# Optimization experiments

Measured on AMD Instinct MI355X. Metric: run time of the kernel, lower is better.

The kernel has to match this reference:

```python
import jax, jax.numpy as jnp
import numpy as np

N_NODES = 100000
N_EDGES = 3200000
N_FEAT = 128
EMBED = 20
N_CLASSES = 10
N_GRAPHS = 64


def setup_inputs() -> dict:
    key = jax.random.key(0)
    ks = jax.random.split(key, 8)
    x = jax.random.normal(ks[0], (N_NODES, N_FEAT), dtype=jnp.float32)
    edge_index = jax.random.randint(ks[1], (2, N_EDGES), 0, N_NODES, dtype=jnp.int64)
    edge_weights = jax.random.uniform(ks[2], (N_EDGES,), dtype=jnp.float32)
    batch = jnp.sort(jax.random.randint(ks[3], (N_NODES,), 0, N_GRAPHS, dtype=jnp.int64))
    # GCNConv parameters (glorot-ish scale) and final linear layer
    W = jax.random.normal(ks[4], (N_FEAT, EMBED), dtype=jnp.float32) * (1.0 / np.sqrt(N_FEAT))
    b = jnp.zeros((EMBED,), dtype=jnp.float32)
    lin_W = jax.random.normal(ks[5], (2 * EMBED, N_CLASSES), dtype=jnp.float32) * (1.0 / np.sqrt(2 * EMBED))
    lin_b = jnp.zeros((N_CLASSES,), dtype=jnp.float32)
    return {"x": x, "edge_index": edge_index, "edge_weights": edge_weights,
            "batch": batch, "W": W, "b": b, "lin_W": lin_W, "lin_b": lin_b}


def reference(x, edge_index, edge_weights, batch, W, b, lin_W, lin_b):
    N = x.shape[0]
    # --- GCNConv with self-loops and symmetric normalization (PyG semantics) ---
    loops = jnp.arange(N, dtype=edge_index.dtype)
    src = jnp.concatenate([edge_index[0], loops])
    dst = jnp.concatenate([edge_index[1], loops])
    w = jnp.concatenate([edge_weights, jnp.ones((N,), dtype=edge_weights.dtype)])
    deg = jax.ops.segment_sum(w, dst, num_segments=N)  # degree at targets
    dinv = jnp.where(deg > 0, jax.lax.rsqrt(deg), 0.0)
    norm = dinv[src] * w * dinv[dst]  # [E+N]
    xw = x @ W  # [N, EMBED]
    msg = xw[src] * norm[:, None]  # gather + scale
    out1 = jax.ops.segment_sum(msg, dst, num_segments=N) + b  # scatter-add
    # --- L2 normalize per node (F.normalize p=2 dim=1, eps=1e-12), then ReLU ---
    nrm = jnp.sqrt(jnp.sum(out1 * out1, axis=1, keepdims=True))
    embed = jax.nn.relu(out1 / jnp.maximum(nrm, 1e-12))
    # --- global max / mean pool per graph ---
    mx = jax.ops.segment_max(embed, batch, num_segments=N_GRAPHS)
    mx = jnp.where(jnp.isfinite(mx), mx, 0.0)  # empty graphs -> 0
    cnt = jax.ops.segment_sum(jnp.ones((N,), dtype=embed.dtype), batch, num_segments=N_GRAPHS)
    mean = jax.ops.segment_sum(embed, batch, num_segments=N_GRAPHS) / jnp.maximum(cnt, 1.0)[:, None]
    pooled = jnp.concatenate([mx, mean], axis=-1)  # [G, 2*EMBED]
    return pooled @ lin_W + lin_b
```

## Files before the change

### kernel.cpp

```cpp
#include <hip/hip_runtime.h>
#include <hip/hip_fp16.h>

#define NN 100000
#define NE 3200000
#define NF 128
#define EM 20
#define NC 10
#define NG 64

#define NB 782
#define CAPB 4608
#define T 4096
#define SBLK 1024

__global__ __launch_bounds__(SBLK) void k_scatter(
        const int* __restrict__ src, const int* __restrict__ dst,
        const float* __restrict__ w, int* __restrict__ gcursor,
        uint2* __restrict__ barr) {
    __shared__ unsigned int cnt[1024];
    __shared__ unsigned int off[1024];
    __shared__ unsigned int gbase[NB];
    __shared__ unsigned int wsum[16];
    __shared__ uint2 staged[T];
    __shared__ unsigned short bkt[T];
    int tid = threadIdx.x;
    long E0 = (long)blockIdx.x * T;
    int tot = (int)min((long)T, (long)NE - E0);
    cnt[tid] = 0;
    __syncthreads();
    unsigned int dreg[T / SBLK];
#pragma unroll
    for (int k = 0; k < T / SBLK; ++k) {
        int e = k * SBLK + tid;
        dreg[k] = 0;
        if (e < tot) {
            dreg[k] = (unsigned)dst[E0 + e];
            atomicAdd(&cnt[dreg[k] >> 7], 1u);
        }
    }
    __syncthreads();
    {
        int lane = tid & 63, wv = tid >> 6;
        unsigned int v = cnt[tid];
        unsigned int s = v;
#pragma unroll
        for (int o = 1; o < 64; o <<= 1) {
            unsigned int t = __shfl_up(s, o);
            if (lane >= o) s += t;
        }
        if (lane == 63) wsum[wv] = s;
        __syncthreads();
        if (tid == 0) {
            unsigned int a = 0;
#pragma unroll
            for (int i = 0; i < 16; ++i) { unsigned int t = wsum[i]; wsum[i] = a; a += t; }
        }
        __syncthreads();
        off[tid] = wsum[wv] + s - v;
    }
    __syncthreads();
    if (tid < NB) {
        unsigned int c = cnt[tid];
        gbase[tid] = c ? (unsigned int)atomicAdd(&gcursor[tid], (int)c) : 0u;
        cnt[tid] = 0;
    }
    __syncthreads();
#pragma unroll
    for (int k = 0; k < T / SBLK; ++k) {
        int e = k * SBLK + tid;
        if (e < tot) {
            long ge = E0 + e;
            unsigned int d = dreg[k];
            unsigned int b = d >> 7;
            unsigned int slot = atomicAdd(&cnt[b], 1u);
            unsigned int pos = off[b] + slot;
            staged[pos] = make_uint2((((unsigned)src[ge]) << 7) | (d & 127u),
                                     __float_as_uint(w[ge]));
            bkt[pos] = (unsigned short)b;
        }
    }
    __syncthreads();
    for (int i = tid; i < tot; i += SBLK) {
        unsigned int b = bkt[i];
        unsigned int gpos = gbase[b] + ((unsigned)i - off[b]);
        if (gpos < CAPB) barr[(size_t)b * CAPB + gpos] = staged[i];
    }
}

__global__ void k_degb(const int* __restrict__ gcursor, const uint2* __restrict__ barr,
                       float* __restrict__ dinv) {
    __shared__ float dacc[128];
    int bk = blockIdx.x, tid = threadIdx.x;
    if (tid < 128) dacc[tid] = 0.f;
    __syncthreads();
    int cntb = min(gcursor[bk], CAPB);
    const uint2* row = barr + (size_t)bk * CAPB;
    for (int i = tid; i < cntb; i += 1024) {
        uint2 r = row[i];
        atomicAdd(&dacc[r.x & 127u], __uint_as_float(r.y));
    }
    __syncthreads();
    if (tid < 128) {
        int gd = bk * 128 + tid;
        if (gd < NN) dinv[gd] = rsqrtf(1.0f + dacc[tid]);
    }
}

__global__ void k_xw(const float* __restrict__ x, const float* __restrict__ W,
                     const float* __restrict__ dinv,
                     __half* __restrict__ xwhA, __half* __restrict__ xwhB) {
    __shared__ float xs[64 * 129];
    __shared__ float Ws[NF * EM];
    int base = blockIdx.x * 64;
    for (int i = threadIdx.x; i < NF * EM; i += 256) Ws[i] = W[i];
    const float4* xg = (const float4*)(x + (size_t)base * NF);
    for (int v = threadIdx.x; v < 64 * NF / 4; v += 256) {
        int fidx = v * 4;
        size_t gidx = (size_t)base * NF + fidx;
        float4 val = (gidx + 3 < (size_t)NN * NF) ? xg[v] : make_float4(0.f, 0.f, 0.f, 0.f);
        int r = fidx / NF, c = fidx % NF;
        float* p = xs + r * 129 + c;
        p[0] = val.x; p[1] = val.y; p[2] = val.z; p[3] = val.w;
    }
    __syncthreads();
    int n = threadIdx.x & 63;
    int jg = threadIdx.x >> 6;
    int j0 = jg * 5;
    if (base + n >= NN) return;
    float acc[5] = {0.f, 0.f, 0.f, 0.f, 0.f};
    const float* xr = xs + n * 129;
#pragma unroll 4
    for (int k = 0; k < NF; ++k) {
        float xv = xr[k];
        const float* wr = Ws + k * EM + j0;
#pragma unroll
        for (int jj = 0; jj < 5; ++jj) acc[jj] = fmaf(xv, wr[jj], acc[jj]);
    }
    float dv = dinv[base + n];
#pragma unroll
    for (int jj = 0; jj < 5; ++jj) {
        int j = j0 + jj;
        __half hv = __float2half(acc[jj] * dv);
        if (j < 16) xwhA[(size_t)(base + n) * 16 + j] = hv;
        else        xwhB[(size_t)(base + n) * 4 + (j - 16)] = hv;
    }
}

__device__ inline void unpack16(uint4 a0, uint4 a1, float* f) {
    const __half2* h = (const __half2*)&a0;
#pragma unroll
    for (int c = 0; c < 4; ++c) { float2 t = __half22float2(h[c]); f[2*c] = t.x; f[2*c+1] = t.y; }
    h = (const __half2*)&a1;
#pragma unroll
    for (int c = 0; c < 4; ++c) { float2 t = __half22float2(h[c]); f[8+2*c] = t.x; f[9+2*c] = t.y; }
}
__device__ inline void unpack4(uint2 b0, float* f) {
    const __half2* h = (const __half2*)&b0;
#pragma unroll
    for (int c = 0; c < 2; ++c) { float2 t = __half22float2(h[c]); f[2*c] = t.x; f[2*c+1] = t.y; }
}

__global__ void k_sortaggr(const int* __restrict__ gcursor,
                           const unsigned long long* __restrict__ barr64,
                           const __half* __restrict__ xwhA, const __half* __restrict__ xwhB,
                           const float* __restrict__ dinv, const float* __restrict__ b,
                           float* __restrict__ embed) {
    __shared__ unsigned long long srt[CAPB];
    __shared__ unsigned int cnt[128];
    __shared__ unsigned int off[128];
    __shared__ unsigned int wtot;
    int bk = blockIdx.x, tid = threadIdx.x;
    if (tid < 128) cnt[tid] = 0;
    __syncthreads();
    int cntb = min(gcursor[bk], CAPB);
    const unsigned long long* row = barr64 + (size_t)bk * CAPB;
    unsigned long long rec[9];
    unsigned int pos[9];
    int K = 0;
    for (int e = tid; e < cntb; e += 512) {
        rec[K] = row[e];
        pos[K] = atomicAdd(&cnt[(unsigned)rec[K] & 127u], 1u);
        ++K;
    }
    __syncthreads();
    unsigned int v = 0, s = 0;
    if (tid < 128) {
        v = cnt[tid]; s = v;
#pragma unroll
        for (int o = 1; o < 64; o <<= 1) {
            unsigned int t = __shfl_up(s, o);
            if ((tid & 63) >= o) s += t;
        }
        if (tid == 63) wtot = s;
    }
    __syncthreads();
    if (tid < 128) {
        if (tid >= 64) s += wtot;
        off[tid] = s;
    }
    __syncthreads();
    for (int k = 0; k < K; ++k) {
        unsigned int dl = (unsigned)rec[k] & 127u;
        srt[off[dl] - cnt[dl] + pos[k]] = rec[k];
    }
    __syncthreads();
    int d = tid >> 2, sub = tid & 3;
    int s0 = (int)(off[d] - cnt[d]), s1 = (int)off[d];
    const uint4* pA = (const uint4*)xwhA;
    const uint2* pB = (const uint2*)xwhB;
    float acc[20];
#pragma unroll
    for (int j = 0; j < 20; ++j) acc[j] = 0.f;
    for (int e = s0 + sub; e < s1; e += 4) {
        unsigned long long r = srt[e];
        unsigned int sN = ((unsigned int)r) >> 7;
        float nw = __uint_as_float((unsigned int)(r >> 32));
        uint4 a0 = pA[(size_t)sN * 2];
        uint4 a1 = pA[(size_t)sN * 2 + 1];
        uint2 b0 = pB[sN];
        float f[20];
        unpack16(a0, a1, f);
        unpack4(b0, f + 16);
#pragma unroll
        for (int j = 0; j < 20; ++j) acc[j] = fmaf(f[j], nw, acc[j]);
    }
#pragma unroll
    for (int j = 0; j < 20; ++j) {
        acc[j] += __shfl_xor(acc[j], 1);
        acc[j] += __shfl_xor(acc[j], 2);
    }
    if (sub == 0) {
        int gd = bk * 128 + d;
        if (gd < NN) {
            float dv = dinv[gd];
            uint4 a0 = pA[(size_t)gd * 2];
            uint4 a1 = pA[(size_t)gd * 2 + 1];
            uint2 b0 = pB[gd];
            float xdh[20];
            unpack16(a0, a1, xdh);
            unpack4(b0, xdh + 16);
            float r[20];
            float ss = 0.f;
#pragma unroll
            for (int j = 0; j < 20; ++j) {
                r[j] = dv * (acc[j] + xdh[j]) + b[j];
                ss = fmaf(r[j], r[j], ss);
            }
            float inv = 1.0f / fmaxf(sqrtf(ss), 1e-12f);
            float4 o4[5];
            float* o = (float*)o4;
#pragma unroll
            for (int j = 0; j < 20; ++j) {
                float e2 = r[j] * inv;
                o[j] = e2 > 0.f ? e2 : 0.f;
            }
            float4* eo = (float4*)(embed + (size_t)gd * EM);
#pragma unroll
            for (int c = 0; c < 5; ++c) eo[c] = o4[c];
        }
    }
}

__device__ inline int lbound(const int* __restrict__ batch, int key) {
    int lo = 0, hi = NN;
    while (lo < hi) {
        int mid = (lo + hi) >> 1;
        if (batch[mid] < key) lo = mid + 1; else hi = mid;
    }
    return lo;
}

__global__ void k_poolfinal(const float* __restrict__ embed, const int* __restrict__ batch,
                            const float* __restrict__ lw, const float* __restrict__ lb,
                            float* __restrict__ out) {
    __shared__ float cross[4][40];
    __shared__ float pooled[40];
    int g = blockIdx.x;
    int s0 = lbound(batch, g), s1 = lbound(batch, g + 1);
    int cnt = s1 - s0;
    float mx[EM], sm[EM];
#pragma unroll
    for (int j = 0; j < EM; ++j) { mx[j] = 0.f; sm[j] = 0.f; }
    for (int n = s0 + threadIdx.x; n < s1; n += 256) {
        const float4* e = (const float4*)(embed + (size_t)n * EM);
#pragma unroll
        for (int c = 0; c < 5; ++c) {
            float4 v = e[c];
            int j = c * 4;
            mx[j+0] = fmaxf(mx[j+0], v.x); sm[j+0] += v.x;
            mx[j+1] = fmaxf(mx[j+1], v.y); sm[j+1] += v.y;
            mx[j+2] = fmaxf(mx[j+2], v.z); sm[j+2] += v.z;
            mx[j+3] = fmaxf(mx[j+3], v.w); sm[j+3] += v.w;
        }
    }
#pragma unroll
    for (int o = 32; o > 0; o >>= 1) {
#pragma unroll
        for (int j = 0; j < EM; ++j) {
            mx[j] = fmaxf(mx[j], __shfl_xor(mx[j], o));
            sm[j] += __shfl_xor(sm[j], o);
        }
    }
    int wave = threadIdx.x >> 6, lane = threadIdx.x & 63;
    if (lane == 0) {
#pragma unroll
        for (int j = 0; j < EM; ++j) { cross[wave][j] = mx[j]; cross[wave][EM + j] = sm[j]; }
    }
    __syncthreads();
    if (threadIdx.x < 40) {
        int j = threadIdx.x;
        float v = cross[0][j];
        if (j < EM) v = fmaxf(fmaxf(v, cross[1][j]), fmaxf(cross[2][j], cross[3][j]));
        else        v = v + cross[1][j] + cross[2][j] + cross[3][j];
        if (j >= EM) v *= 1.0f / fmaxf((float)cnt, 1.0f);
        pooled[j] = v;
    }
    __syncthreads();
    if (threadIdx.x < NC) {
        int c = threadIdx.x;
        float acc = lb[c];
#pragma unroll
        for (int j = 0; j < 2 * EM; ++j) acc = fmaf(pooled[j], lw[j * NC + c], acc);
        out[g * NC + c] = acc;
    }
}

static inline size_t align_up(size_t v) { return (v + 1023) & ~(size_t)1023; }

extern "C" void kernel_launch(void* const* d_in, const int* in_sizes, int n_in,
                              void* d_out, int out_size, void* d_ws, size_t ws_size,
                              hipStream_t stream) {
    const float* x     = (const float*)d_in[0];
    const int*   ei    = (const int*)d_in[1];
    const float* ew    = (const float*)d_in[2];
    const int*   batch = (const int*)d_in[3];
    const float* W     = (const float*)d_in[4];
    const float* b     = (const float*)d_in[5];
    const float* lw    = (const float*)d_in[6];
    const float* lb    = (const float*)d_in[7];
    float* out = (float*)d_out;

    char* ws = (char*)d_ws;
    int*    gcursor = (int*)ws;    ws += align_up(4096);
    float*  dinv    = (float*)ws;  ws += align_up((size_t)NN * 4);
    __half* xwhA    = (__half*)ws; ws += align_up((size_t)NN * 16 * 2);
    __half* xwhB    = (__half*)ws; ws += align_up((size_t)NN * 4 * 2);
    float*  embed   = (float*)ws;  ws += align_up((size_t)NN * EM * 4);
    uint2*  barr    = (uint2*)ws;
    unsigned long long* barr64 = (unsigned long long*)barr;

    const int* srcp = ei;
    const int* dstp = ei + NE;

    (void)hipMemsetAsync(gcursor, 0, 4096, stream);
    k_scatter<<<(NE + T - 1) / T, SBLK, 0, stream>>>(srcp, dstp, ew, gcursor, barr);
    k_degb<<<NB, 1024, 0, stream>>>(gcursor, barr, dinv);
    k_xw<<<(NN + 63) / 64, 256, 0, stream>>>(x, W, dinv, xwhA, xwhB);
    k_sortaggr<<<NB, 512, 0, stream>>>(gcursor, barr64, xwhA, xwhB, dinv, b, embed);
    k_poolfinal<<<NG, 256, 0, stream>>>(embed, batch, lw, lb, out);
}
```

Measured before the change: 266.0 us.

## Move per-bucket counting sort into degree kernel, slim aggregation kernel

The counting sort of bucket records by local destination moves from the aggregation kernel into the degree kernel. That kernel now writes the sorted records back to global memory along with per-destination row pointers, and computes degrees by summing sorted weights serially. The aggregation kernel then reads sorted records directly from global memory and skips all LDS sorting, which should cut its shared memory use and raise occupancy. The cost is an extra global write of the bucket array, a serial per-destination degree loop, and a log-step scan that uses many block barriers.

```diff
diff --git a/kernel.cpp b/kernel.cpp
--- a/kernel.cpp
+++ b/kernel.cpp
@@ -87,22 +87,51 @@
     }
 }
 
-__global__ void k_degb(const int* __restrict__ gcursor, const uint2* __restrict__ barr,
-                       float* __restrict__ dinv) {
-    __shared__ float dacc[128];
+__global__ __launch_bounds__(1024) void k_sortb(const int* __restrict__ gcursor,
+                                                unsigned long long* __restrict__ barr64,
+                                                int* __restrict__ rowptrs,
+                                                float* __restrict__ dinv) {
+    __shared__ unsigned long long srt[CAPB];
+    __shared__ unsigned int cnt[128];
+    __shared__ unsigned int off[128];
     int bk = blockIdx.x, tid = threadIdx.x;
-    if (tid < 128) dacc[tid] = 0.f;
+    if (tid < 128) cnt[tid] = 0;
     __syncthreads();
     int cntb = min(gcursor[bk], CAPB);
-    const uint2* row = barr + (size_t)bk * CAPB;
-    for (int i = tid; i < cntb; i += 1024) {
-        uint2 r = row[i];
-        atomicAdd(&dacc[r.x & 127u], __uint_as_float(r.y));
-    }
-    __syncthreads();
+    unsigned long long* row = barr64 + (size_t)bk * CAPB;
+    unsigned long long rec[5];
+    unsigned int pos[5];
+    int K = 0;
+    for (int e = tid; e < cntb; e += 1024) {
+        rec[K] = row[e];
+        pos[K] = atomicAdd(&cnt[(unsigned)rec[K] & 127u], 1u);
+        ++K;
+    }
+    __syncthreads();
+    if (tid < 128) off[tid] = cnt[tid];
+    __syncthreads();
+    for (int d = 1; d < 128; d <<= 1) {
+        unsigned int v = 0;
+        if (tid < 128 && tid >= (unsigned)d) v = off[tid - d];
+        __syncthreads();
+        if (tid < 128 && tid >= (unsigned)d) off[tid] += v;
+        __syncthreads();
+    }
+    for (int k = 0; k < K; ++k) {
+        unsigned int dl = (unsigned)rec[k] & 127u;
+        srt[off[dl] - cnt[dl] + pos[k]] = rec[k];
+    }
+    __syncthreads();
+    for (int e = tid; e < cntb; e += 1024) row[e] = srt[e];
+    if (tid < 128) rowptrs[bk * 129 + tid] = (int)(off[tid] - cnt[tid]);
+    if (tid == 0) rowptrs[bk * 129 + 128] = cntb;
     if (tid < 128) {
+        unsigned int s0 = off[tid] - cnt[tid], s1 = off[tid];
+        float s = 1.0f;
+        for (unsigned int i = s0; i < s1; ++i)
+            s += __uint_as_float((unsigned int)(srt[i] >> 32));
         int gd = bk * 128 + tid;
-        if (gd < NN) dinv[gd] = rsqrtf(1.0f + dacc[tid]);
+        if (gd < NN) dinv[gd] = rsqrtf(s);
     }
 }
 
@@ -160,59 +189,22 @@
     for (int c = 0; c < 2; ++c) { float2 t = __half22float2(h[c]); f[2*c] = t.x; f[2*c+1] = t.y; }
 }
 
-__global__ void k_sortaggr(const int* __restrict__ gcursor,
-                           const unsigned long long* __restrict__ barr64,
-                           const __half* __restrict__ xwhA, const __half* __restrict__ xwhB,
-                           const float* __restrict__ dinv, const float* __restrict__ b,
-                           float* __restrict__ embed) {
-    __shared__ unsigned long long srt[CAPB];
-    __shared__ unsigned int cnt[128];
-    __shared__ unsigned int off[128];
-    __shared__ unsigned int wtot;
+__global__ __launch_bounds__(512) void k_aggr(
+        const int* __restrict__ rowptrs, const unsigned long long* __restrict__ barr64,
+        const __half* __restrict__ xwhA, const __half* __restrict__ xwhB,
+        const float* __restrict__ dinv, const float* __restrict__ b,
+        float* __restrict__ embed) {
     int bk = blockIdx.x, tid = threadIdx.x;
-    if (tid < 128) cnt[tid] = 0;
-    __syncthreads();
-    int cntb = min(gcursor[bk], CAPB);
+    int d = tid >> 2, sub = tid & 3;
+    int s0 = rowptrs[bk * 129 + d], s1 = rowptrs[bk * 129 + d + 1];
     const unsigned long long* row = barr64 + (size_t)bk * CAPB;
-    unsigned long long rec[9];
-    unsigned int pos[9];
-    int K = 0;
-    for (int e = tid; e < cntb; e += 512) {
-        rec[K] = row[e];
-        pos[K] = atomicAdd(&cnt[(unsigned)rec[K] & 127u], 1u);
-        ++K;
-    }
-    __syncthreads();
-    unsigned int v = 0, s = 0;
-    if (tid < 128) {
-        v = cnt[tid]; s = v;
-#pragma unroll
-        for (int o = 1; o < 64; o <<= 1) {
-            unsigned int t = __shfl_up(s, o);
-            if ((tid & 63) >= o) s += t;
-        }
-        if (tid == 63) wtot = s;
-    }
-    __syncthreads();
-    if (tid < 128) {
-        if (tid >= 64) s += wtot;
-        off[tid] = s;
-    }
-    __syncthreads();
-    for (int k = 0; k < K; ++k) {
-        unsigned int dl = (unsigned)rec[k] & 127u;
-        srt[off[dl] - cnt[dl] + pos[k]] = rec[k];
-    }
-    __syncthreads();
-    int d = tid >> 2, sub = tid & 3;
-    int s0 = (int)(off[d] - cnt[d]), s1 = (int)off[d];
     const uint4* pA = (const uint4*)xwhA;
     const uint2* pB = (const uint2*)xwhB;
     float acc[20];
 #pragma unroll
     for (int j = 0; j < 20; ++j) acc[j] = 0.f;
     for (int e = s0 + sub; e < s1; e += 4) {
-        unsigned long long r = srt[e];
+        unsigned long long r = row[e];
         unsigned int sN = ((unsigned int)r) >> 7;
         float nw = __uint_as_float((unsigned int)(r >> 32));
         uint4 a0 = pA[(size_t)sN * 2];
@@ -342,6 +334,7 @@
 
     char* ws = (char*)d_ws;
     int*    gcursor = (int*)ws;    ws += align_up(4096);
+    int*    rowptrs = (int*)ws;    ws += align_up((size_t)NB * 129 * 4);
     float*  dinv    = (float*)ws;  ws += align_up((size_t)NN * 4);
     __half* xwhA    = (__half*)ws; ws += align_up((size_t)NN * 16 * 2);
     __half* xwhB    = (__half*)ws; ws += align_up((size_t)NN * 4 * 2);
@@ -354,8 +347,8 @@
 
     (void)hipMemsetAsync(gcursor, 0, 4096, stream);
     k_scatter<<<(NE + T - 1) / T, SBLK, 0, stream>>>(srcp, dstp, ew, gcursor, barr);
-    k_degb<<<NB, 1024, 0, stream>>>(gcursor, barr, dinv);
+    k_sortb<<<NB, 1024, 0, stream>>>(gcursor, barr64, rowptrs, dinv);
     k_xw<<<(NN + 63) / 64, 256, 0, stream>>>(x, W, dinv, xwhA, xwhB);
-    k_sortaggr<<<NB, 512, 0, stream>>>(gcursor, barr64, xwhA, xwhB, dinv, b, embed);
+    k_aggr<<<NB, 512, 0, stream>>>(rowptrs, barr64, xwhA, xwhB, dinv, b, embed);
     k_poolfinal<<<NG, 256, 0, stream>>>(embed, batch, lw, lb, out);
 }
```

Result: no change. 269.2 us (+1.2%).

## Fuse all GCN stages into one persistent cooperative kernel with grid syncs

Applied to the files above, without the earlier changes.

Merges the memset, scatter, degree, xW, sort-aggregate and pool kernels into a single cooperative kernel that loops over tiles persistently, with grid.sync between phases. The scatter block shrinks from 1024 to 512 threads with a multi-pass shared-memory scan, and the sort phase now keeps per-edge ranks in shared memory and rereads records instead of holding them in registers. The aim is to remove launch gaps and the separate memset. The cost is grid-wide barriers, a grid bounded by occupancy, and serialized phases that leave little room for overlap.

```diff
diff --git a/kernel.cpp b/kernel.cpp
--- a/kernel.cpp
+++ b/kernel.cpp
@@ -1,5 +1,8 @@
 #include <hip/hip_runtime.h>
 #include <hip/hip_fp16.h>
+#include <hip/hip_cooperative_groups.h>
+
+namespace cg = cooperative_groups;
 
 #define NN 100000
 #define NE 3200000
@@ -11,140 +14,23 @@
 #define NB 782
 #define CAPB 4608
 #define T 4096
-#define SBLK 1024
-
-__global__ __launch_bounds__(SBLK) void k_scatter(
-        const int* __restrict__ src, const int* __restrict__ dst,
-        const float* __restrict__ w, int* __restrict__ gcursor,
-        uint2* __restrict__ barr) {
-    __shared__ unsigned int cnt[1024];
-    __shared__ unsigned int off[1024];
-    __shared__ unsigned int gbase[NB];
-    __shared__ unsigned int wsum[16];
-    __shared__ uint2 staged[T];
-    __shared__ unsigned short bkt[T];
-    int tid = threadIdx.x;
-    long E0 = (long)blockIdx.x * T;
-    int tot = (int)min((long)T, (long)NE - E0);
-    cnt[tid] = 0;
-    __syncthreads();
-    unsigned int dreg[T / SBLK];
-#pragma unroll
-    for (int k = 0; k < T / SBLK; ++k) {
-        int e = k * SBLK + tid;
-        dreg[k] = 0;
-        if (e < tot) {
-            dreg[k] = (unsigned)dst[E0 + e];
-            atomicAdd(&cnt[dreg[k] >> 7], 1u);
-        }
-    }
-    __syncthreads();
-    {
-        int lane = tid & 63, wv = tid >> 6;
-        unsigned int v = cnt[tid];
-        unsigned int s = v;
-#pragma unroll
-        for (int o = 1; o < 64; o <<= 1) {
-            unsigned int t = __shfl_up(s, o);
-            if (lane >= o) s += t;
-        }
-        if (lane == 63) wsum[wv] = s;
-        __syncthreads();
-        if (tid == 0) {
-            unsigned int a = 0;
-#pragma unroll
-            for (int i = 0; i < 16; ++i) { unsigned int t = wsum[i]; wsum[i] = a; a += t; }
-        }
-        __syncthreads();
-        off[tid] = wsum[wv] + s - v;
-    }
-    __syncthreads();
-    if (tid < NB) {
-        unsigned int c = cnt[tid];
-        gbase[tid] = c ? (unsigned int)atomicAdd(&gcursor[tid], (int)c) : 0u;
-        cnt[tid] = 0;
-    }
-    __syncthreads();
-#pragma unroll
-    for (int k = 0; k < T / SBLK; ++k) {
-        int e = k * SBLK + tid;
-        if (e < tot) {
-            long ge = E0 + e;
-            unsigned int d = dreg[k];
-            unsigned int b = d >> 7;
-            unsigned int slot = atomicAdd(&cnt[b], 1u);
-            unsigned int pos = off[b] + slot;
-            staged[pos] = make_uint2((((unsigned)src[ge]) << 7) | (d & 127u),
-                                     __float_as_uint(w[ge]));
-            bkt[pos] = (unsigned short)b;
-        }
-    }
-    __syncthreads();
-    for (int i = tid; i < tot; i += SBLK) {
-        unsigned int b = bkt[i];
-        unsigned int gpos = gbase[b] + ((unsigned)i - off[b]);
-        if (gpos < CAPB) barr[(size_t)b * CAPB + gpos] = staged[i];
-    }
-}
-
-__global__ void k_degb(const int* __restrict__ gcursor, const uint2* __restrict__ barr,
-                       float* __restrict__ dinv) {
-    __shared__ float dacc[128];
-    int bk = blockIdx.x, tid = threadIdx.x;
-    if (tid < 128) dacc[tid] = 0.f;
-    __syncthreads();
-    int cntb = min(gcursor[bk], CAPB);
-    const uint2* row = barr + (size_t)bk * CAPB;
-    for (int i = tid; i < cntb; i += 1024) {
-        uint2 r = row[i];
-        atomicAdd(&dacc[r.x & 127u], __uint_as_float(r.y));
-    }
-    __syncthreads();
-    if (tid < 128) {
-        int gd = bk * 128 + tid;
-        if (gd < NN) dinv[gd] = rsqrtf(1.0f + dacc[tid]);
-    }
-}
-
-__global__ void k_xw(const float* __restrict__ x, const float* __restrict__ W,
-                     const float* __restrict__ dinv,
-                     __half* __restrict__ xwhA, __half* __restrict__ xwhB) {
-    __shared__ float xs[64 * 129];
-    __shared__ float Ws[NF * EM];
-    int base = blockIdx.x * 64;
-    for (int i = threadIdx.x; i < NF * EM; i += 256) Ws[i] = W[i];
-    const float4* xg = (const float4*)(x + (size_t)base * NF);
-    for (int v = threadIdx.x; v < 64 * NF / 4; v += 256) {
-        int fidx = v * 4;
-        size_t gidx = (size_t)base * NF + fidx;
-        float4 val = (gidx + 3 < (size_t)NN * NF) ? xg[v] : make_float4(0.f, 0.f, 0.f, 0.f);
-        int r = fidx / NF, c = fidx % NF;
-        float* p = xs + r * 129 + c;
-        p[0] = val.x; p[1] = val.y; p[2] = val.z; p[3] = val.w;
-    }
-    __syncthreads();
-    int n = threadIdx.x & 63;
-    int jg = threadIdx.x >> 6;
-    int j0 = jg * 5;
-    if (base + n >= NN) return;
-    float acc[5] = {0.f, 0.f, 0.f, 0.f, 0.f};
-    const float* xr = xs + n * 129;
-#pragma unroll 4
-    for (int k = 0; k < NF; ++k) {
-        float xv = xr[k];
-        const float* wr = Ws + k * EM + j0;
-#pragma unroll
-        for (int jj = 0; jj < 5; ++jj) acc[jj] = fmaf(xv, wr[jj], acc[jj]);
-    }
-    float dv = dinv[base + n];
-#pragma unroll
-    for (int jj = 0; jj < 5; ++jj) {
-        int j = j0 + jj;
-        __half hv = __float2half(acc[jj] * dv);
-        if (j < 16) xwhA[(size_t)(base + n) * 16 + j] = hv;
-        else        xwhB[(size_t)(base + n) * 4 + (j - 16)] = hv;
-    }
-}
+#define NTILES ((NE + T - 1) / T)
+#define XTILES ((NN + 63) / 64)
+#define BLK 512
+
+#define L_CNT    0
+#define L_OFF    4096
+#define L_GBASE  8192
+#define L_WSUM   12288
+#define L_STAGED 12352
+#define L_BKT    45120
+#define S_SRT    0
+#define S_CNT    36864
+#define S_OFF    37376
+#define S_RANK   37888
+#define S_WTOT   47104
+#define X_WS     0
+#define X_XS     10240
 
 __device__ inline void unpack16(uint4 a0, uint4 a1, float* f) {
     const __half2* h = (const __half2*)&a0;
@@ -159,108 +45,6 @@
 #pragma unroll
     for (int c = 0; c < 2; ++c) { float2 t = __half22float2(h[c]); f[2*c] = t.x; f[2*c+1] = t.y; }
 }
-
-__global__ void k_sortaggr(const int* __restrict__ gcursor,
-                           const unsigned long long* __restrict__ barr64,
-                           const __half* __restrict__ xwhA, const __half* __restrict__ xwhB,
-                           const float* __restrict__ dinv, const float* __restrict__ b,
-                           float* __restrict__ embed) {
-    __shared__ unsigned long long srt[CAPB];
-    __shared__ unsigned int cnt[128];
-    __shared__ unsigned int off[128];
-    __shared__ unsigned int wtot;
-    int bk = blockIdx.x, tid = threadIdx.x;
-    if (tid < 128) cnt[tid] = 0;
-    __syncthreads();
-    int cntb = min(gcursor[bk], CAPB);
-    const unsigned long long* row = barr64 + (size_t)bk * CAPB;
-    unsigned long long rec[9];
-    unsigned int pos[9];
-    int K = 0;
-    for (int e = tid; e < cntb; e += 512) {
-        rec[K] = row[e];
-        pos[K] = atomicAdd(&cnt[(unsigned)rec[K] & 127u], 1u);
-        ++K;
-    }
-    __syncthreads();
-    unsigned int v = 0, s = 0;
-    if (tid < 128) {
-        v = cnt[tid]; s = v;
-#pragma unroll
-        for (int o = 1; o < 64; o <<= 1) {
-            unsigned int t = __shfl_up(s, o);
-            if ((tid & 63) >= o) s += t;
-        }
-        if (tid == 63) wtot = s;
-    }
-    __syncthreads();
-    if (tid < 128) {
-        if (tid >= 64) s += wtot;
-        off[tid] = s;
-    }
-    __syncthreads();
-    for (int k = 0; k < K; ++k) {
-        unsigned int dl = (unsigned)rec[k] & 127u;
-        srt[off[dl] - cnt[dl] + pos[k]] = rec[k];
-    }
-    __syncthreads();
-    int d = tid >> 2, sub = tid & 3;
-    int s0 = (int)(off[d] - cnt[d]), s1 = (int)off[d];
-    const uint4* pA = (const uint4*)xwhA;
-    const uint2* pB = (const uint2*)xwhB;
-    float acc[20];
-#pragma unroll
-    for (int j = 0; j < 20; ++j) acc[j] = 0.f;
-    for (int e = s0 + sub; e < s1; e += 4) {
-        unsigned long long r = srt[e];
-        unsigned int sN = ((unsigned int)r) >> 7;
-        float nw = __uint_as_float((unsigned int)(r >> 32));
-        uint4 a0 = pA[(size_t)sN * 2];
-        uint4 a1 = pA[(size_t)sN * 2 + 1];
-        uint2 b0 = pB[sN];
-        float f[20];
-        unpack16(a0, a1, f);
-        unpack4(b0, f + 16);
-#pragma unroll
-        for (int j = 0; j < 20; ++j) acc[j] = fmaf(f[j], nw, acc[j]);
-    }
-#pragma unroll
-    for (int j = 0; j < 20; ++j) {
-        acc[j] += __shfl_xor(acc[j], 1);
-        acc[j] += __shfl_xor(acc[j], 2);
-    }
-    if (sub == 0) {
-        int gd = bk * 128 + d;
-        if (gd < NN) {
-            float dv = dinv[gd];
-            uint4 a0 = pA[(size_t)gd * 2];
-            uint4 a1 = pA[(size_t)gd * 2 + 1];
-            uint2 b0 = pB[gd];
-            float xdh[20];
-            unpack16(a0, a1, xdh);
-            unpack4(b0, xdh + 16);
-            float r[20];
-            float ss = 0.f;
-#pragma unroll
-            for (int j = 0; j < 20; ++j) {
-                r[j] = dv * (acc[j] + xdh[j]) + b[j];
-                ss = fmaf(r[j], r[j], ss);
-            }
-            float inv = 1.0f / fmaxf(sqrtf(ss), 1e-12f);
-            float4 o4[5];
-            float* o = (float*)o4;
-#pragma unroll
-            for (int j = 0; j < 20; ++j) {
-                float e2 = r[j] * inv;
-                o[j] = e2 > 0.f ? e2 : 0.f;
-            }
-            float4* eo = (float4*)(embed + (size_t)gd * EM);
-#pragma unroll
-            for (int c = 0; c < 5; ++c) eo[c] = o4[c];
-        }
-    }
-}
-
 __device__ inline int lbound(const int* __restrict__ batch, int key) {
     int lo = 0, hi = NN;
     while (lo < hi) {
@@ -270,58 +54,308 @@
     return lo;
 }
 
-__global__ void k_poolfinal(const float* __restrict__ embed, const int* __restrict__ batch,
-                            const float* __restrict__ lw, const float* __restrict__ lb,
-                            float* __restrict__ out) {
-    __shared__ float cross[4][40];
-    __shared__ float pooled[40];
-    int g = blockIdx.x;
-    int s0 = lbound(batch, g), s1 = lbound(batch, g + 1);
-    int cnt = s1 - s0;
-    float mx[EM], sm[EM];
-#pragma unroll
-    for (int j = 0; j < EM; ++j) { mx[j] = 0.f; sm[j] = 0.f; }
-    for (int n = s0 + threadIdx.x; n < s1; n += 256) {
-        const float4* e = (const float4*)(embed + (size_t)n * EM);
-#pragma unroll
-        for (int c = 0; c < 5; ++c) {
-            float4 v = e[c];
-            int j = c * 4;
-            mx[j+0] = fmaxf(mx[j+0], v.x); sm[j+0] += v.x;
-            mx[j+1] = fmaxf(mx[j+1], v.y); sm[j+1] += v.y;
-            mx[j+2] = fmaxf(mx[j+2], v.z); sm[j+2] += v.z;
-            mx[j+3] = fmaxf(mx[j+3], v.w); sm[j+3] += v.w;
+__global__ __launch_bounds__(BLK) void k_fused(
+        const int* __restrict__ src, const int* __restrict__ dst,
+        const float* __restrict__ ew, const float* __restrict__ x,
+        const float* __restrict__ W, const float* __restrict__ b,
+        const float* __restrict__ lw, const float* __restrict__ lb,
+        const int* __restrict__ batch, float* __restrict__ out,
+        int* __restrict__ gcursor, float* __restrict__ dinv,
+        __half* __restrict__ xwhA, __half* __restrict__ xwhB,
+        float* __restrict__ embed, unsigned long long* __restrict__ barr) {
+    cg::grid_group grid = cg::this_grid();
+    __shared__ __align__(16) unsigned char L[53312];
+    int tid = threadIdx.x;
+
+    if (blockIdx.x == 0)
+        for (int i = tid; i < 1024; i += BLK) gcursor[i] = 0;
+    grid.sync();
+
+    {
+        unsigned int* cnt   = (unsigned int*)(L + L_CNT);
+        unsigned int* off   = (unsigned int*)(L + L_OFF);
+        unsigned int* gbase = (unsigned int*)(L + L_GBASE);
+        unsigned long long* staged = (unsigned long long*)(L + L_STAGED);
+        unsigned short* bkt = (unsigned short*)(L + L_BKT);
+        unsigned int* scratch = (unsigned int*)staged;
+        for (int tile = blockIdx.x; tile < NTILES; tile += gridDim.x) {
+            long E0 = (long)tile * T;
+            int tot = (int)min((long)T, (long)NE - E0);
+            for (int i = tid; i < 1024; i += BLK) { cnt[i] = 0; scratch[i] = 0; }
+            __syncthreads();
+            for (int k = 0; k < T / BLK; ++k) {
+                int e = k * BLK + tid;
+                if (e < tot) atomicAdd(&cnt[((unsigned)dst[E0 + e]) >> 7], 1u);
+            }
+            __syncthreads();
+            for (int i = tid; i < 1024; i += BLK) scratch[i] = cnt[i];
+            __syncthreads();
+            for (int d = 1; d < 1024; d <<= 1) {
+                unsigned int v[2];
+#pragma unroll
+                for (int q = 0; q < 2; ++q) {
+                    int idx = q * BLK + tid;
+                    v[q] = (idx >= d) ? scratch[idx - d] : 0u;
+                }
+                __syncthreads();
+#pragma unroll
+                for (int q = 0; q < 2; ++q) scratch[q * BLK + tid] += v[q];
+                __syncthreads();
+            }
+            for (int i = tid; i < 1024; i += BLK) off[i] = scratch[i] - cnt[i];
+            __syncthreads();
+            for (int i = tid; i < NB; i += BLK) {
+                unsigned int c = cnt[i];
+                gbase[i] = c ? (unsigned int)atomicAdd(&gcursor[i], (int)c) : 0u;
+                cnt[i] = 0;
+            }
+            __syncthreads();
+            for (int k = 0; k < T / BLK; ++k) {
+                int e = k * BLK + tid;
+                if (e < tot) {
+                    long ge = E0 + e;
+                    unsigned int d = (unsigned)dst[ge];
+                    unsigned int bb = d >> 7;
+                    unsigned int slot = atomicAdd(&cnt[bb], 1u);
+                    unsigned int pos = off[bb] + slot;
+                    unsigned long long rec = ((unsigned long long)__float_as_uint(ew[ge]) << 32)
+                                           | ((((unsigned)src[ge]) << 7) | (d & 127u));
+                    staged[pos] = rec;
+                    bkt[pos] = (unsigned short)bb;
+                }
+            }
+            __syncthreads();
+            for (int i = tid; i < tot; i += BLK) {
+                unsigned int bb = bkt[i];
+                unsigned int gpos = gbase[bb] + ((unsigned)i - off[bb]);
+                if (gpos < CAPB) barr[(size_t)bb * CAPB + gpos] = staged[i];
+            }
+            __syncthreads();
         }
     }
-#pragma unroll
-    for (int o = 32; o > 0; o >>= 1) {
-#pragma unroll
-        for (int j = 0; j < EM; ++j) {
-            mx[j] = fmaxf(mx[j], __shfl_xor(mx[j], o));
-            sm[j] += __shfl_xor(sm[j], o);
+    __threadfence();
+    grid.sync();
+
+    {
+        float* dacc = (float*)L;
+        for (int bk = blockIdx.x; bk < NB; bk += gridDim.x) {
+            if (tid < 128) dacc[tid] = 0.f;
+            __syncthreads();
+            int cntb = min(gcursor[bk], CAPB);
+            const unsigned long long* row = barr + (size_t)bk * CAPB;
+            for (int i = tid; i < cntb; i += BLK) {
+                unsigned long long r = row[i];
+                atomicAdd(&dacc[(unsigned)r & 127u], __uint_as_float((unsigned)(r >> 32)));
+            }
+            __syncthreads();
+            if (tid < 128) {
+                int gd = bk * 128 + tid;
+                if (gd < NN) dinv[gd] = rsqrtf(1.0f + dacc[tid]);
+            }
+            __syncthreads();
         }
     }
-    int wave = threadIdx.x >> 6, lane = threadIdx.x & 63;
-    if (lane == 0) {
-#pragma unroll
-        for (int j = 0; j < EM; ++j) { cross[wave][j] = mx[j]; cross[wave][EM + j] = sm[j]; }
-    }
-    __syncthreads();
-    if (threadIdx.x < 40) {
-        int j = threadIdx.x;
-        float v = cross[0][j];
-        if (j < EM) v = fmaxf(fmaxf(v, cross[1][j]), fmaxf(cross[2][j], cross[3][j]));
-        else        v = v + cross[1][j] + cross[2][j] + cross[3][j];
-        if (j >= EM) v *= 1.0f / fmaxf((float)cnt, 1.0f);
-        pooled[j] = v;
-    }
-    __syncthreads();
-    if (threadIdx.x < NC) {
-        int c = threadIdx.x;
-        float acc = lb[c];
-#pragma unroll
-        for (int j = 0; j < 2 * EM; ++j) acc = fmaf(pooled[j], lw[j * NC + c], acc);
-        out[g * NC + c] = acc;
+    __threadfence();
+    grid.sync();
+
+    {
+        float* Ws = (float*)(L + X_WS);
+        float* xs = (float*)(L + X_XS);
+        for (int i = tid; i < NF * EM; i += BLK) Ws[i] = W[i];
+        for (int t = blockIdx.x; t < XTILES; t += gridDim.x) {
+            int base = t * 64;
+            __syncthreads();
+            const float4* xg = (const float4*)(x + (size_t)base * NF);
+            for (int v = tid; v < 64 * NF / 4; v += BLK) {
+                int fidx = v * 4;
+                size_t gidx = (size_t)base * NF + fidx;
+                float4 val = (gidx + 3 < (size_t)NN * NF) ? xg[v] : make_float4(0.f, 0.f, 0.f, 0.f);
+                int r = fidx / NF, c = fidx % NF;
+                float* p = xs + r * 129 + c;
+                p[0] = val.x; p[1] = val.y; p[2] = val.z; p[3] = val.w;
+            }
+            __syncthreads();
+            if (tid < 256) {
+                int n = tid & 63;
+                int jg = tid >> 6;
+                int j0 = jg * 5;
+                if (base + n < NN) {
+                    float acc[5] = {0.f, 0.f, 0.f, 0.f, 0.f};
+                    const float* xr = xs + n * 129;
+#pragma unroll 4
+                    for (int k = 0; k < NF; ++k) {
+                        float xv = xr[k];
+                        const float* wr = Ws + k * EM + j0;
+#pragma unroll
+                        for (int jj = 0; jj < 5; ++jj) acc[jj] = fmaf(xv, wr[jj], acc[jj]);
+                    }
+                    float dv = dinv[base + n];
+#pragma unroll
+                    for (int jj = 0; jj < 5; ++jj) {
+                        int j = j0 + jj;
+                        __half hv = __float2half(acc[jj] * dv);
+                        if (j < 16) xwhA[(size_t)(base + n) * 16 + j] = hv;
+                        else        xwhB[(size_t)(base + n) * 4 + (j - 16)] = hv;
+                    }
+                }
+            }
+        }
+    }
+    __threadfence();
+    grid.sync();
+
+    {
+        unsigned long long* srt = (unsigned long long*)(L + S_SRT);
+        unsigned int* cnt2 = (unsigned int*)(L + S_CNT);
+        unsigned int* off2 = (unsigned int*)(L + S_OFF);
+        unsigned short* rank = (unsigned short*)(L + S_RANK);
+        unsigned int* wtot = (unsigned int*)(L + S_WTOT);
+        const uint4* pA = (const uint4*)xwhA;
+        const uint2* pB = (const uint2*)xwhB;
+        for (int bk = blockIdx.x; bk < NB; bk += gridDim.x) {
+            if (tid < 128) cnt2[tid] = 0;
+            __syncthreads();
+            int cntb = min(gcursor[bk], CAPB);
+            const unsigned long long* row = barr + (size_t)bk * CAPB;
+            for (int e = tid; e < cntb; e += BLK)
+                rank[e] = (unsigned short)atomicAdd(&cnt2[(unsigned)row[e] & 127u], 1u);
+            __syncthreads();
+            unsigned int v = 0, s = 0;
+            if (tid < 128) {
+                v = cnt2[tid]; s = v;
+#pragma unroll
+                for (int o = 1; o < 64; o <<= 1) {
+                    unsigned int t2 = __shfl_up(s, o);
+                    if ((tid & 63) >= o) s += t2;
+                }
+                if (tid == 63) *wtot = s;
+            }
+            __syncthreads();
+            if (tid < 128) {
+                if (tid >= 64) s += *wtot;
+                off2[tid] = s;
+            }
+            __syncthreads();
+            for (int e = tid; e < cntb; e += BLK) {
+                unsigned long long r = row[e];
+                unsigned int dl = (unsigned)r & 127u;
+                srt[off2[dl] - cnt2[dl] + rank[e]] = r;
+            }
+            __syncthreads();
+            int d = tid >> 2, sub = tid & 3;
+            int s0 = (int)(off2[d] - cnt2[d]), s1 = (int)off2[d];
+            float acc[20];
+#pragma unroll
+            for (int j = 0; j < 20; ++j) acc[j] = 0.f;
+            for (int e = s0 + sub; e < s1; e += 4) {
+                unsigned long long r = srt[e];
+                unsigned int sN = ((unsigned)r) >> 7;
+                float nw = __uint_as_float((unsigned)(r >> 32));
+                uint4 a0 = pA[(size_t)sN * 2];
+                uint4 a1 = pA[(size_t)sN * 2 + 1];
+                uint2 b0 = pB[sN];
+                float f[20];
+                unpack16(a0, a1, f);
+                unpack4(b0, f + 16);
+#pragma unroll
+                for (int j = 0; j < 20; ++j) acc[j] = fmaf(f[j], nw, acc[j]);
+            }
+#pragma unroll
+            for (int j = 0; j < 20; ++j) {
+                acc[j] += __shfl_xor(acc[j], 1);
+                acc[j] += __shfl_xor(acc[j], 2);
+            }
+            if (sub == 0) {
+                int gd = bk * 128 + d;
+                if (gd < NN) {
+                    float dv = dinv[gd];
+                    uint4 a0 = pA[(size_t)gd * 2];
+                    uint4 a1 = pA[(size_t)gd * 2 + 1];
+                    uint2 b0 = pB[gd];
+                    float xdh[20];
+                    unpack16(a0, a1, xdh);
+                    unpack4(b0, xdh + 16);
+                    float r[20];
+                    float ss = 0.f;
+#pragma unroll
+                    for (int j = 0; j < 20; ++j) {
+                        r[j] = dv * (acc[j] + xdh[j]) + b[j];
+                        ss = fmaf(r[j], r[j], ss);
+                    }
+                    float inv = 1.0f / fmaxf(sqrtf(ss), 1e-12f);
+                    float4 o4[5];
+                    float* o = (float*)o4;
+#pragma unroll
+                    for (int j = 0; j < 20; ++j) {
+                        float e2 = r[j] * inv;
+                        o[j] = e2 > 0.f ? e2 : 0.f;
+                    }
+                    float4* eo = (float4*)(embed + (size_t)gd * EM);
+#pragma unroll
+                    for (int c = 0; c < 5; ++c) eo[c] = o4[c];
+                }
+            }
+            __syncthreads();
+        }
+    }
+    __threadfence();
+    grid.sync();
+
+    {
+        float (*cross)[40] = (float(*)[40])L;
+        float* pooled = (float*)(L + 4 * 40 * 4);
+        for (int g = blockIdx.x; g < NG; g += gridDim.x) {
+            int s0 = lbound(batch, g), s1 = lbound(batch, g + 1);
+            int cntg = s1 - s0;
+            if (tid < 256) {
+                float mx[EM], sm[EM];
+#pragma unroll
+                for (int j = 0; j < EM; ++j) { mx[j] = 0.f; sm[j] = 0.f; }
+                for (int n = s0 + tid; n < s1; n += 256) {
+                    const float4* e = (const float4*)(embed + (size_t)n * EM);
+#pragma unroll
+                    for (int c = 0; c < 5; ++c) {
+                        float4 v = e[c];
+                        int j = c * 4;
+                        mx[j+0] = fmaxf(mx[j+0], v.x); sm[j+0] += v.x;
+                        mx[j+1] = fmaxf(mx[j+1], v.y); sm[j+1] += v.y;
+                        mx[j+2] = fmaxf(mx[j+2], v.z); sm[j+2] += v.z;
+                        mx[j+3] = fmaxf(mx[j+3], v.w); sm[j+3] += v.w;
+                    }
+                }
+#pragma unroll
+                for (int o = 32; o > 0; o >>= 1) {
+#pragma unroll
+                    for (int j = 0; j < EM; ++j) {
+                        mx[j] = fmaxf(mx[j], __shfl_xor(mx[j], o));
+                        sm[j] += __shfl_xor(sm[j], o);
+                    }
+                }
+                int wave = tid >> 6, lane = tid & 63;
+                if (lane == 0) {
+#pragma unroll
+                    for (int j = 0; j < EM; ++j) { cross[wave][j] = mx[j]; cross[wave][EM + j] = sm[j]; }
+                }
+            }
+            __syncthreads();
+            if (tid < 40) {
+                int j = tid;
+                float v = cross[0][j];
+                if (j < EM) v = fmaxf(fmaxf(v, cross[1][j]), fmaxf(cross[2][j], cross[3][j]));
+                else        v = v + cross[1][j] + cross[2][j] + cross[3][j];
+                if (j >= EM) v *= 1.0f / fmaxf((float)cntg, 1.0f);
+                pooled[j] = v;
+            }
+            __syncthreads();
+            if (tid < NC) {
+                int c = tid;
+                float acc = lb[c];
+#pragma unroll
+                for (int j = 0; j < 2 * EM; ++j) acc = fmaf(pooled[j], lw[j * NC + c], acc);
+                out[g * NC + c] = acc;
+            }
+            __syncthreads();
+        }
     }
 }
 
@@ -330,8 +364,10 @@
 extern "C" void kernel_launch(void* const* d_in, const int* in_sizes, int n_in,
                               void* d_out, int out_size, void* d_ws, size_t ws_size,
                               hipStream_t stream) {
+    const int*   ei    = (const int*)d_in[1];
+    const int*   srcp  = ei;
+    const int*   dstp  = ei + NE;
     const float* x     = (const float*)d_in[0];
-    const int*   ei    = (const int*)d_in[1];
     const float* ew    = (const float*)d_in[2];
     const int*   batch = (const int*)d_in[3];
     const float* W     = (const float*)d_in[4];
@@ -346,16 +382,19 @@
     __half* xwhA    = (__half*)ws; ws += align_up((size_t)NN * 16 * 2);
     __half* xwhB    = (__half*)ws; ws += align_up((size_t)NN * 4 * 2);
     float*  embed   = (float*)ws;  ws += align_up((size_t)NN * EM * 4);
-    uint2*  barr    = (uint2*)ws;
-    unsigned long long* barr64 = (unsigned long long*)barr;
-
-    const int* srcp = ei;
-    const int* dstp = ei + NE;
-
-    (void)hipMemsetAsync(gcursor, 0, 4096, stream);
-    k_scatter<<<(NE + T - 1) / T, SBLK, 0, stream>>>(srcp, dstp, ew, gcursor, barr);
-    k_degb<<<NB, 1024, 0, stream>>>(gcursor, barr, dinv);
-    k_xw<<<(NN + 63) / 64, 256, 0, stream>>>(x, W, dinv, xwhA, xwhB);
-    k_sortaggr<<<NB, 512, 0, stream>>>(gcursor, barr64, xwhA, xwhB, dinv, b, embed);
-    k_poolfinal<<<NG, 256, 0, stream>>>(embed, batch, lw, lb, out);
+    unsigned long long* barr64 = (unsigned long long*)ws;
+
+    int occ = 0;
+    (void)hipOccupancyMaxActiveBlocksPerMultiprocessor(&occ, k_fused, BLK, 0);
+    if (occ < 1) occ = 1;
+    int grid = occ * 256;
+    if (grid > 2048) grid = 2048;
+
+    void* args[] = { (void*)&srcp, (void*)&dstp, (void*)&ew, (void*)&x,
+                     (void*)&W, (void*)&b, (void*)&lw, (void*)&lb,
+                     (void*)&batch, (void*)&out,
+                     (void*)&gcursor, (void*)&dinv, (void*)&xwhA, (void*)&xwhB,
+                     (void*)&embed, (void*)&barr64 };
+    (void)hipLaunchCooperativeKernel((const void*)k_fused, dim3(grid), dim3(BLK),
+                                     args, 0, stream);
 }
```

Measured after the change: 646.6 us. +143.1%, slower.
